# Performance work log

Hardware: AMD Instinct MI355X
Metric: run time of the kernel (lower is better)

Reference implementation:

```python
import jax, jax.numpy as jnp
import numpy as np

GRID_SIZE = 5
NUM_BASES = 2 ** GRID_SIZE - 1  # 31: actual number of Haar bases produced by the loop

def _haar_edges():
    left, mid, right = [], [], []
    for level in range(GRID_SIZE):
        scale = 2 ** level
        for shift in range(scale):
            left.append(shift / scale)
            mid.append((shift + 0.5) / scale)
            right.append((shift + 1.0) / scale)
    return (np.asarray(left, np.float32), np.asarray(mid, np.float32), np.asarray(right, np.float32))

_LEFT, _MID, _RIGHT = _haar_edges()


def setup_inputs() -> dict:
    key = jax.random.key(0)
    k1, k2, k3 = jax.random.split(key, 3)
    B, IN, OUT = 16384, 256, 256
    x = jax.random.normal(k1, (B, IN), dtype=jnp.float32)
    base_weight = jax.random.normal(k2, (OUT, IN), dtype=jnp.float32) * 0.05
    spline_weight = jax.random.normal(k3, (OUT, IN, NUM_BASES), dtype=jnp.float32) * 0.05
    spline_scaler = jnp.ones((OUT, IN), dtype=jnp.float32)
    return {"x": x, "base_weight": base_weight, "spline_weight": spline_weight, "spline_scaler": spline_scaler}


def reference(x, base_weight, spline_weight, spline_scaler):
    # per-feature min/max normalization over the batch dim
    x_min = jnp.min(x, axis=0, keepdims=True)
    x_max = jnp.max(x, axis=0, keepdims=True)
    xn = (x - x_min) / (x_max - x_min + 1e-8)            # [B, IN]
    left = jnp.asarray(_LEFT, x.dtype)
    mid = jnp.asarray(_MID, x.dtype)
    right = jnp.asarray(_RIGHT, x.dtype)
    xe = xn[..., None]                                    # [B, IN, 1]
    mask1 = ((xe >= left) & (xe < mid)).astype(x.dtype)
    mask2 = ((xe >= mid) & (xe < right)).astype(x.dtype)
    bases = mask1 - mask2                                 # [B, IN, NB]
    base_out = jax.nn.relu(x) @ base_weight.T             # [B, OUT]
    sw = spline_weight * spline_scaler[..., None]         # [OUT, IN, NB]
    wavelet_out = jnp.einsum('bik,oik->bo', bases, sw)    # [B, OUT]
    return base_out + wavelet_out
```

## Files before the change

kernel.cpp:

```cpp
#include <hip/hip_runtime.h>
#include <stdint.h>

typedef short s16x8 __attribute__((ext_vector_type(8)));
typedef float f32x4 __attribute__((ext_vector_type(4)));

#define IN_F   256
#define OUT_F  256
#define BATCH  16384
#define NB     31
#define KONE   8192
#define KTOT   8448

typedef const __attribute__((address_space(1))) void* as1cvp;
typedef __attribute__((address_space(3))) void* as3vp;

__device__ __forceinline__ unsigned short f2bf(float f) {
    unsigned u = __float_as_uint(f);
    u += 0x7FFFu + ((u >> 16) & 1u);
    return (unsigned short)(u >> 16);
}
__device__ __forceinline__ unsigned fkey(float f) {
    unsigned b = __float_as_uint(f);
    return (b & 0x80000000u) ? ~b : (b | 0x80000000u);
}
__device__ __forceinline__ float funkey(unsigned k) {
    return __uint_as_float((k & 0x80000000u) ? (k & 0x7FFFFFFFu) : ~k);
}

__global__ void minmax_atomic(const float* __restrict__ x,
                              unsigned* __restrict__ pminP, unsigned* __restrict__ pmaxP) {
    const int t = threadIdx.x;
    const int b0 = blockIdx.x * 32;
    float mn = 3.4e38f, mx = -3.4e38f;
    for (int r = 0; r < 32; ++r) {
        float v = x[(size_t)(b0 + r) * IN_F + t];
        mn = fminf(mn, v);
        mx = fmaxf(mx, v);
    }
    atomicMin(&pminP[t], fkey(mn));
    atomicMax(&pmaxP[t], fkey(mx));
}

__global__ void build_wb(const float* __restrict__ bw, const float* __restrict__ sw,
                         const float* __restrict__ sc, unsigned short* __restrict__ Wb) {
    const int o = blockIdx.x;
    const int k0 = blockIdx.y * 2112;
    const int t = threadIdx.x;
    for (int k = k0 + t; k < k0 + 2112; k += 256) {
        float val;
        if (k < KONE) {
            int i = k >> 5, j = k & 31;
            float s = sc[o * IN_F + i];
            float acc = 0.f;
#pragma unroll
            for (int l = 0; l < 5; ++l) {
                int kk = (1 << l) - 1 + (j >> (5 - l));
                float w = sw[((size_t)(o * IN_F + i)) * NB + kk];
                acc += (((j >> (4 - l)) & 1) ? -w : w);
            }
            val = acc * s;
        } else {
            val = bw[o * IN_F + (k - KONE)];
        }
        Wb[(size_t)o * KTOT + k] = f2bf(val);
    }
}

__global__ __launch_bounds__(256) void leafk_t(
    const float* __restrict__ x, const unsigned* __restrict__ pminP,
    const unsigned* __restrict__ pmaxP, unsigned char* __restrict__ lt) {
    __shared__ unsigned char lsh[256 * 68];
    __shared__ float xminsh[IN_F], rdensh[IN_F];
    const int t = threadIdx.x;
    const int b0 = blockIdx.x * 64;
    {
        float mn = funkey(pminP[t]), mx = funkey(pmaxP[t]);
        xminsh[t] = mn;
        rdensh[t] = 1.0f / (mx - mn + 1e-8f);
    }
    __syncthreads();
    const float xmn = xminsh[t], rdn = rdensh[t];
    for (int r = 0; r < 64; ++r) {
        float v = x[(size_t)(b0 + r) * IN_F + t];
        float xn = (v - xmn) * rdn;
        int l = (int)(xn * 32.0f);
        lsh[t * 68 + r] = (l >= 0 && l < 32) ? (unsigned char)l : (unsigned char)255;
    }
    __syncthreads();
    const int lane = t & 63, w = t >> 6;
    const unsigned* lshU = (const unsigned*)lsh;
#pragma unroll
    for (int ib = 0; ib < 16; ++ib) {
        int i = ib * 16 + w * 4 + (lane >> 4);
        unsigned val = lshU[i * 17 + (lane & 15)];
        *(unsigned*)(lt + (size_t)i * BATCH + b0 + (lane & 15) * 4) = val;
    }
}

__global__ __launch_bounds__(128, 2) void gemm_kan(
    const float* __restrict__ x,
    const unsigned short* __restrict__ Wb,
    const unsigned char* __restrict__ lt,
    float* __restrict__ out)
{
    __shared__ unsigned short Ash[64 * 64];
    __shared__ unsigned short Bsh[2 * 64 * 64];

    const int t     = threadIdx.x;
    const int lane  = t & 63;
    const int wv    = t >> 6;
    const int mtile = blockIdx.x;
    const int ntile = blockIdx.y;

    {
        uint4 z; z.x = z.y = z.z = z.w = 0u;
        uint4* a4 = (uint4*)Ash;
#pragma unroll
        for (int r = 0; r < 4; ++r) a4[t + r * 128] = z;
    }

    const unsigned char* bbase = (const unsigned char*)(Wb
        + (size_t)(ntile * 64 + wv * 32 + (lane >> 3)) * KTOT
        + (((lane & 7) ^ (lane >> 3)) << 3));

    const int am = t >> 1;
    const int ag = t & 1;
    const size_t lrow0 = (size_t)mtile * 64;
    int ps = -1;

    unsigned char lf = lt[(size_t)ag * BATCH + lrow0 + am];

#pragma unroll
    for (int q = 0; q < 4; ++q)
        __builtin_amdgcn_global_load_lds(
            (as1cvp)(bbase + (size_t)q * 8 * KTOT * 2),
            (as3vp)(uint32_t)(uintptr_t)(Bsh + wv * 2048 + q * 512), 16, 0, 0);
    __syncthreads();

    f32x4 acc[2][4] = {};
    const int rr = lane & 15, kq = lane >> 4;

    for (int kb = 0; kb < 132; ++kb) {
        const int cur = kb & 1;
        if (kb < 128) {
            if (ps >= 0) Ash[ps] = 0;
            int l = lf;
            if (l < 32) {
                int c = (ag << 2) + (l >> 3);
                ps = (am << 6) + ((c ^ (am & 7)) << 3) + (l & 7);
                Ash[ps] = 0x3F80;
            } else ps = -1;
        } else {
            const float* xr = x + (size_t)(mtile * 64 + wv * 32) * IN_F + (kb - 128) * 64 + lane;
            const int cslot = (lane >> 3);
#pragma unroll
            for (int m0 = 0; m0 < 32; ++m0) {
                int m = wv * 32 + m0;
                float v = xr[(size_t)m0 * IN_F];
                Ash[(m << 6) + ((cslot ^ (m & 7)) << 3) + (lane & 7)] = f2bf(fmaxf(v, 0.0f));
            }
        }
        __syncthreads();

        if (kb + 1 < 132) {
            const unsigned char* src = bbase + (size_t)(kb + 1) * 128;
            unsigned short* dst = Bsh + (1 - cur) * 4096 + wv * 2048;
#pragma unroll
            for (int q = 0; q < 4; ++q)
                __builtin_amdgcn_global_load_lds(
                    (as1cvp)(src + (size_t)q * 8 * KTOT * 2),
                    (as3vp)(uint32_t)(uintptr_t)(dst + q * 512), 16, 0, 0);
        }
        if (kb + 1 < 128) {
            lf = lt[(size_t)((kb + 1) * 2 + ag) * BATCH + lrow0 + am];
        }

        const unsigned short* bb = Bsh + cur * 4096;
#pragma unroll
        for (int ks = 0; ks < 2; ++ks) {
            const int c = (ks << 2) + kq;
            s16x8 af[2], bfr[4];
#pragma unroll
            for (int mt = 0; mt < 2; ++mt) {
                int m = wv * 32 + mt * 16 + rr;
                af[mt] = *(const s16x8*)&Ash[(m << 6) + ((c ^ (m & 7)) << 3)];
            }
#pragma unroll
            for (int nt = 0; nt < 4; ++nt) {
                int n = nt * 16 + rr;
                bfr[nt] = *(const s16x8*)&bb[(n << 6) + ((c ^ (n & 7)) << 3)];
            }
#pragma unroll
            for (int mt = 0; mt < 2; ++mt)
#pragma unroll
                for (int nt = 0; nt < 4; ++nt)
                    acc[mt][nt] = __builtin_amdgcn_mfma_f32_16x16x32_bf16(
                        af[mt], bfr[nt], acc[mt][nt], 0, 0, 0);
        }
        __syncthreads();
    }

    const int rq = lane >> 4;
#pragma unroll
    for (int mt = 0; mt < 2; ++mt)
#pragma unroll
        for (int nt = 0; nt < 4; ++nt)
#pragma unroll
            for (int v = 0; v < 4; ++v) {
                int row = mtile * 64 + wv * 32 + mt * 16 + rq * 4 + v;
                int col = ntile * 64 + nt * 16 + rr;
                out[(size_t)row * OUT_F + col] = acc[mt][nt][v];
            }
}

extern "C" void kernel_launch(void* const* d_in, const int* in_sizes, int n_in,
                              void* d_out, int out_size, void* d_ws, size_t ws_size,
                              hipStream_t stream) {
    (void)in_sizes; (void)n_in; (void)out_size; (void)ws_size;
    const float* x  = (const float*)d_in[0];
    const float* bw = (const float*)d_in[1];
    const float* sw = (const float*)d_in[2];
    const float* sc = (const float*)d_in[3];
    float* out = (float*)d_out;

    char* ws = (char*)d_ws;
    unsigned short* Wb   = (unsigned short*)ws;
    unsigned char*  lt   = (unsigned char*)(ws + 4325376);
    unsigned*       pminP = (unsigned*)(ws + 8519680);
    unsigned*       pmaxP = (unsigned*)(ws + 8520704);

    hipMemsetAsync(pminP, 0xFF, 1024, stream);
    hipMemsetAsync(pmaxP, 0x00, 1024, stream);

    minmax_atomic<<<512, 256, 0, stream>>>(x, pminP, pmaxP);
    build_wb<<<dim3(256, 4), 256, 0, stream>>>(bw, sw, sc, Wb);
    leafk_t<<<256, 256, 0, stream>>>(x, pminP, pmaxP, lt);
    gemm_kan<<<dim3(256, 4), 128, 0, stream>>>(x, Wb, lt, out);
}
```

Baseline: 179.6 us.

## Fuse min/max and weight-build prep kernels, drop atomics, remove redundant GEMM barrier

The separate min/max kernel, the weight-building kernel and the two memsets become one prep kernel. Its first 256 blocks write per-block partial min/max values, and the remaining blocks build the fused bf16 weight row for each (o,i) pair. Each thread loads the 31 spline weights once and stores them as 16-byte vectors. The leaf kernel now reduces those partials itself instead of reading atomically merged keys. In the GEMM, each wave zeroes and uses only its own A-tile rows, so the barrier between the A writes and the MFMA reads is removed. The cost is that every leaf block redundantly reduces 256 partials, and correctness now depends on the A tile staying wave-private.

```diff
diff --git a/kernel.cpp b/kernel.cpp
--- a/kernel.cpp
+++ b/kernel.cpp
@@ -19,67 +19,73 @@
     u += 0x7FFFu + ((u >> 16) & 1u);
     return (unsigned short)(u >> 16);
 }
-__device__ __forceinline__ unsigned fkey(float f) {
-    unsigned b = __float_as_uint(f);
-    return (b & 0x80000000u) ? ~b : (b | 0x80000000u);
-}
-__device__ __forceinline__ float funkey(unsigned k) {
-    return __uint_as_float((k & 0x80000000u) ? (k & 0x7FFFFFFFu) : ~k);
-}
-
-__global__ void minmax_atomic(const float* __restrict__ x,
-                              unsigned* __restrict__ pminP, unsigned* __restrict__ pmaxP) {
+
+__global__ __launch_bounds__(256) void prep1(
+    const float* __restrict__ x, const float* __restrict__ bw,
+    const float* __restrict__ sw, const float* __restrict__ sc,
+    float* __restrict__ pmn, float* __restrict__ pmx,
+    unsigned short* __restrict__ Wb) {
+    const int blk = blockIdx.x, t = threadIdx.x;
+    if (blk < 256) {
+        const int b0 = blk * 64;
+        float mn = 3.4e38f, mx = -3.4e38f;
+        for (int r = 0; r < 64; ++r) {
+            float v = x[(size_t)(b0 + r) * IN_F + t];
+            mn = fminf(mn, v);
+            mx = fmaxf(mx, v);
+        }
+        pmn[blk * 256 + t] = mn;
+        pmx[blk * 256 + t] = mx;
+    } else {
+        const int o = blk - 256, i = t;
+        const float s = sc[o * IN_F + i];
+        const float* swp = sw + (size_t)(o * IN_F + i) * NB;
+        float w[NB];
+#pragma unroll
+        for (int k = 0; k < NB; ++k) w[k] = swp[k];
+        unsigned short* dst = Wb + (size_t)o * KTOT + i * 32;
+#pragma unroll
+        for (int q = 0; q < 4; ++q) {
+            union { s16x8 v; unsigned short s8[8]; } pk;
+#pragma unroll
+            for (int e = 0; e < 8; ++e) {
+                int j = q * 8 + e;
+                float acc = 0.f;
+#pragma unroll
+                for (int l = 0; l < 5; ++l) {
+                    int kk = (1 << l) - 1 + (j >> (5 - l));
+                    acc += (((j >> (4 - l)) & 1) ? -w[kk] : w[kk]);
+                }
+                pk.s8[e] = f2bf(acc * s);
+            }
+            *(s16x8*)(dst + q * 8) = pk.v;
+        }
+        Wb[(size_t)o * KTOT + KONE + i] = f2bf(bw[o * IN_F + i]);
+    }
+}
+
+__global__ __launch_bounds__(256) void leaf2t(
+    const float* __restrict__ x, const float* __restrict__ pmn,
+    const float* __restrict__ pmx, unsigned char* __restrict__ lt) {
+    __shared__ unsigned char lsh[256 * 68];
+    __shared__ float xminsh[IN_F], rdnsh[IN_F];
     const int t = threadIdx.x;
-    const int b0 = blockIdx.x * 32;
-    float mn = 3.4e38f, mx = -3.4e38f;
-    for (int r = 0; r < 32; ++r) {
-        float v = x[(size_t)(b0 + r) * IN_F + t];
-        mn = fminf(mn, v);
-        mx = fmaxf(mx, v);
-    }
-    atomicMin(&pminP[t], fkey(mn));
-    atomicMax(&pmaxP[t], fkey(mx));
-}
-
-__global__ void build_wb(const float* __restrict__ bw, const float* __restrict__ sw,
-                         const float* __restrict__ sc, unsigned short* __restrict__ Wb) {
-    const int o = blockIdx.x;
-    const int k0 = blockIdx.y * 2112;
-    const int t = threadIdx.x;
-    for (int k = k0 + t; k < k0 + 2112; k += 256) {
-        float val;
-        if (k < KONE) {
-            int i = k >> 5, j = k & 31;
-            float s = sc[o * IN_F + i];
-            float acc = 0.f;
-#pragma unroll
-            for (int l = 0; l < 5; ++l) {
-                int kk = (1 << l) - 1 + (j >> (5 - l));
-                float w = sw[((size_t)(o * IN_F + i)) * NB + kk];
-                acc += (((j >> (4 - l)) & 1) ? -w : w);
-            }
-            val = acc * s;
-        } else {
-            val = bw[o * IN_F + (k - KONE)];
-        }
-        Wb[(size_t)o * KTOT + k] = f2bf(val);
-    }
-}
-
-__global__ __launch_bounds__(256) void leafk_t(
-    const float* __restrict__ x, const unsigned* __restrict__ pminP,
-    const unsigned* __restrict__ pmaxP, unsigned char* __restrict__ lt) {
-    __shared__ unsigned char lsh[256 * 68];
-    __shared__ float xminsh[IN_F], rdensh[IN_F];
-    const int t = threadIdx.x;
+    {
+        float mn0 = 3.4e38f, mn1 = 3.4e38f, mx0 = -3.4e38f, mx1 = -3.4e38f;
+#pragma unroll 8
+        for (int b = 0; b < 256; b += 2) {
+            mn0 = fminf(mn0, pmn[(size_t)b * 256 + t]);
+            mn1 = fminf(mn1, pmn[(size_t)(b + 1) * 256 + t]);
+            mx0 = fmaxf(mx0, pmx[(size_t)b * 256 + t]);
+            mx1 = fmaxf(mx1, pmx[(size_t)(b + 1) * 256 + t]);
+        }
+        float mn = fminf(mn0, mn1), mx = fmaxf(mx0, mx1);
+        xminsh[t] = mn;
+        rdnsh[t] = 1.0f / (mx - mn + 1e-8f);
+    }
+    __syncthreads();
+    const float xmn = xminsh[t], rdn = rdnsh[t];
     const int b0 = blockIdx.x * 64;
-    {
-        float mn = funkey(pminP[t]), mx = funkey(pmaxP[t]);
-        xminsh[t] = mn;
-        rdensh[t] = 1.0f / (mx - mn + 1e-8f);
-    }
-    __syncthreads();
-    const float xmn = xminsh[t], rdn = rdensh[t];
     for (int r = 0; r < 64; ++r) {
         float v = x[(size_t)(b0 + r) * IN_F + t];
         float xn = (v - xmn) * rdn;
@@ -114,9 +120,9 @@
 
     {
         uint4 z; z.x = z.y = z.z = z.w = 0u;
-        uint4* a4 = (uint4*)Ash;
-#pragma unroll
-        for (int r = 0; r < 4; ++r) a4[t + r * 128] = z;
+        uint4* a4 = (uint4*)(Ash + wv * 2048);
+#pragma unroll
+        for (int r = 0; r < 4; ++r) a4[lane + r * 64] = z;
     }
 
     const unsigned char* bbase = (const unsigned char*)(Wb
@@ -160,7 +166,6 @@
                 Ash[(m << 6) + ((cslot ^ (m & 7)) << 3) + (lane & 7)] = f2bf(fmaxf(v, 0.0f));
             }
         }
-        __syncthreads();
 
         if (kb + 1 < 132) {
             const unsigned char* src = bbase + (size_t)(kb + 1) * 128;
@@ -224,16 +229,12 @@
     float* out = (float*)d_out;
 
     char* ws = (char*)d_ws;
-    unsigned short* Wb   = (unsigned short*)ws;
-    unsigned char*  lt   = (unsigned char*)(ws + 4325376);
-    unsigned*       pminP = (unsigned*)(ws + 8519680);
-    unsigned*       pmaxP = (unsigned*)(ws + 8520704);
-
-    hipMemsetAsync(pminP, 0xFF, 1024, stream);
-    hipMemsetAsync(pmaxP, 0x00, 1024, stream);
-
-    minmax_atomic<<<512, 256, 0, stream>>>(x, pminP, pmaxP);
-    build_wb<<<dim3(256, 4), 256, 0, stream>>>(bw, sw, sc, Wb);
-    leafk_t<<<256, 256, 0, stream>>>(x, pminP, pmaxP, lt);
+    unsigned short* Wb = (unsigned short*)ws;
+    unsigned char*  lt = (unsigned char*)(ws + 4325376);
+    float* pmn = (float*)(ws + 8519680);
+    float* pmx = (float*)(ws + 8781824);
+
+    prep1<<<512, 256, 0, stream>>>(x, bw, sw, sc, pmn, pmx, Wb);
+    leaf2t<<<256, 256, 0, stream>>>(x, pmn, pmx, lt);
     gemm_kan<<<dim3(256, 4), 128, 0, stream>>>(x, Wb, lt, out);
 }
```

Result: faster. 168.4 us (-6.3%).
